# Kernel tuning notes

Measured on AMD Instinct MI355X. Metric: run time of the kernel, lower is better.

The kernel has to match this reference:

```python
import jax, jax.numpy as jnp
import numpy as np

B, S, D, H, C, E, V = 8, 2048, 1024, 512, 256, 64, 64


def setup_inputs() -> dict:
    key = jax.random.key(0)
    ks = jax.random.split(key, 40)
    ri = lambda i, hi: jax.random.randint(ks[i], (B, S), 0, hi).astype(jnp.int32)
    p = lambda i, shape: (jax.random.normal(ks[i], shape, jnp.float32) * 0.02)
    inp = {
        'h_x': jax.random.normal(ks[0], (B, S, D), jnp.float32),
        'h_y': jax.random.normal(ks[1], (B, S, D), jnp.float32),
        'x_mask': jnp.ones((B, S), jnp.int32),
        'y_mask': jnp.ones((B, S), jnp.int32),
        'src_token_dense_mask': ri(2, 2), 'src_token_sparse_mask': ri(3, 2),
        'src_token_inarc_type': ri(4, V), 'src_token_arc_head': ri(5, S),
        'src_token_depth': ri(6, 16), 'src_word_inarc_type': ri(7, V),
        'src_word_inarc_type_mask': ri(8, 2),
        'tgt_token_dense_mask': ri(9, 2), 'tgt_token_sparse_mask': ri(10, 2),
        'tgt_token_inarc_type': ri(11, V), 'tgt_token_arc_head': ri(12, S),
        'tgt_token_depth': ri(13, 16), 'tgt_word_inarc_type': ri(14, V),
        'tgt_word_inarc_type_mask': ri(15, 2),
        # src MLP [D->H->C], tgt MLP [D->H->C]
        'W1s': p(16, (D, H)), 'b1s': jnp.zeros((H,), jnp.float32),
        'W2s': p(17, (H, C)), 'b2s': jnp.zeros((C,), jnp.float32),
        'W1t': p(18, (D, H)), 'b1t': jnp.zeros((H,), jnp.float32),
        'W2t': p(19, (H, C)), 'b2t': jnp.zeros((C,), jnp.float32),
        # inarc edge embedding + GeneralConv params
        'emb': p(20, (V, E)),
        'W_msg': p(21, (C, C)), 'b_msg': jnp.zeros((C,), jnp.float32),
        'W_edge': p(22, (E, C)),
        'att': p(23, (C,)),
        'W_self': p(24, (C, C)), 'b_self': jnp.zeros((C,), jnp.float32),
        # axis_feature MLP [C->C]
        'Wf': p(25, (C, C)), 'bf': jnp.zeros((C,), jnp.float32),
    }
    return inp


def _mlp(h, W1, b1, W2, b2):
    return jax.nn.leaky_relu(h @ W1 + b1) @ W2 + b2


def _graph_side(h, dense_m, sparse_m, arc_head, word_type, word_mask,
                W1, b1, W2, b2, emb, W_msg, b_msg, W_edge, att, W_self, b_self, Wf, bf):
    Bn, Sn, _ = h.shape
    x = _mlp(h, W1, b1, W2, b2)                      # [B,S,C]
    N = Bn * Sn
    Cn = x.shape[-1]
    xg = x.reshape(N, Cn)                            # debatch -> nodes
    off = (jnp.arange(Bn, dtype=jnp.int32) * Sn)[:, None]
    src = (arc_head + off).reshape(N)                # global head index per token
    dst = jnp.arange(N, dtype=jnp.int32)             # one in-edge per token
    valid = (sparse_m * dense_m).reshape(N).astype(x.dtype)
    ef = emb[(word_type * word_mask).reshape(N)]     # [N,E] edge embeddings
    # GeneralConv: directed message with edge features + additive attention
    m = xg[src] @ W_msg + b_msg + ef @ W_edge        # [N,C] messages
    hd = xg @ W_msg + b_msg                          # dst-side term for attention
    logit = jax.nn.leaky_relu(((m + hd) * att).sum(-1))
    logit = jnp.where(valid > 0, logit, -1e9)
    emax = jax.ops.segment_max(logit, dst, num_segments=N)
    ex = jnp.exp(logit - emax[dst]) * valid
    den = jax.ops.segment_sum(ex, dst, num_segments=N)
    alpha = ex / (den[dst] + 1e-16)                  # softmax per destination node
    agg = jax.ops.segment_sum(m * alpha[:, None], dst, num_segments=N)
    out = xg @ W_self + b_self + agg                 # skip_linear
    out = out / jnp.maximum(jnp.linalg.norm(out, axis=-1, keepdims=True), 1e-12)
    r = out.reshape(Bn, Sn, Cn).mean(axis=1, keepdims=True)  # FeatureRepr mean
    return r @ Wf + bf                               # [B,1,C]


def reference(h_x, x_mask, src_token_dense_mask, src_token_sparse_mask,
              src_token_inarc_type, src_token_arc_head, src_token_depth,
              src_word_inarc_type, src_word_inarc_type_mask,
              h_y, y_mask, tgt_token_dense_mask, tgt_token_sparse_mask,
              tgt_token_inarc_type, tgt_token_arc_head, tgt_token_depth,
              tgt_word_inarc_type, tgt_word_inarc_type_mask,
              W1s, b1s, W2s, b2s, W1t, b1t, W2t, b2t,
              emb, W_msg, b_msg, W_edge, att, W_self, b_self, Wf, bf):
    src_repr = _graph_side(h_x, src_token_dense_mask, src_token_sparse_mask,
                           src_token_arc_head, src_word_inarc_type, src_word_inarc_type_mask,
                           W1s, b1s, W2s, b2s, emb, W_msg, b_msg, W_edge, att,
                           W_self, b_self, Wf, bf)
    tgt_repr = _graph_side(h_y, tgt_token_dense_mask, tgt_token_sparse_mask,
                           tgt_token_arc_head, tgt_word_inarc_type, tgt_word_inarc_type_mask,
                           W1t, b1t, W2t, b2t, emb, W_msg, b_msg, W_edge, att,
                           W_self, b_self, Wf, bf)
    return (src_repr, tgt_repr)
```

## Files before the change

### kernel.cpp

```cpp
#include <hip/hip_runtime.h>
#include <stdint.h>

#define SEQ   2048
#define NNODE 16384

typedef short  short8  __attribute__((ext_vector_type(8)));
typedef float  float4v __attribute__((ext_vector_type(4)));
typedef unsigned short u16;
typedef unsigned short u16x8 __attribute__((ext_vector_type(8)));
typedef short  short4v __attribute__((ext_vector_type(4)));

__device__ __forceinline__ float b2f(u16 u) {
    union { unsigned int i; float f; } x; x.i = ((unsigned int)u) << 16; return x.f;
}
__device__ __forceinline__ u16 f2b(float f) {
    union { float f; unsigned int i; } x; x.f = f;
    unsigned int u = x.i;
    unsigned int r = (u + 0x7fffu + ((u >> 16) & 1u)) >> 16;
    return (u16)r;
}

__device__ __forceinline__ void gld16(const void* g, void* l) {
    __builtin_amdgcn_global_load_lds(
        (const __attribute__((address_space(1))) void*)g,
        (__attribute__((address_space(3))) void*)l, 16, 0, 0);
}

struct GemmP {
    const void*  A[2];
    const u16*   B[2];
    const float* bias[2];
    u16*         out[2];
};

template <int MB>
__device__ __forceinline__ void mfma4(const short8* af, const short8* bq,
                                      float4v (*acc)[4]) {
#pragma unroll
    for (int mi = 0; mi < 4; ++mi)
#pragma unroll
        for (int ni = 0; ni < 4; ++ni)
            acc[MB + mi][ni] = __builtin_amdgcn_mfma_f32_16x16x32_bf16(
                af[mi], bq[ni], acc[MB + mi][ni], 0, 0, 0);
}

#define TILE_BODY(AC, BC, KN, AG, BG, ACV, PL, PC)                            \
    {                                                                         \
        short8 bq[4], af[4];                                                  \
        _Pragma("unroll") for (int ni = 0; ni < 4; ++ni)                      \
            bq[ni] = *(const short8*)((BC) + boff + ni * 512);                \
        _Pragma("unroll") for (int mi = 0; mi < 4; ++mi)                      \
            af[mi] = *(const short8*)((AC) + aoff + mi * 512);                \
        if constexpr (AF32) prefA32(KN, PL); else stageA16(KN, AG);           \
        __builtin_amdgcn_s_barrier();                                         \
        __builtin_amdgcn_s_setprio(1);                                        \
        mfma4<0>(af, bq, acc);                                                \
        __builtin_amdgcn_s_setprio(0);                                        \
        __builtin_amdgcn_s_barrier();                                         \
        _Pragma("unroll") for (int mi = 0; mi < 4; ++mi)                      \
            af[mi] = *(const short8*)((AC) + aoff + (4 + mi) * 512);          \
        stageB(KN, BG);                                                       \
        if constexpr (AF32) {                                                 \
            cvtWrite(PC, ACV);                                                \
            asm volatile("s_waitcnt lgkmcnt(0)" ::: "memory");                \
            asm volatile("s_waitcnt vmcnt(6)" ::: "memory");                  \
        } else {                                                              \
            asm volatile("s_waitcnt vmcnt(4)" ::: "memory");                  \
        }                                                                     \
        __builtin_amdgcn_s_barrier();                                         \
        __builtin_amdgcn_s_setprio(1);                                        \
        mfma4<4>(af, bq, acc);                                                \
        __builtin_amdgcn_s_setprio(0);                                        \
        __builtin_amdgcn_s_barrier();                                         \
    }

template <int ACT, int AF32>
__global__ __launch_bounds__(512, 2) void gemm8_k(GemmP p, int M, int N, int K) {
    __shared__ __align__(16) u16 smem[49152];

    const int z = blockIdx.z;
    const u16*   __restrict__ Bg   = p.B[z];
    const float* __restrict__ bias = p.bias[z];
    const u16*   __restrict__ A16  = (const u16*)p.A[z];
    const float* __restrict__ A32  = (const float*)p.A[z];

    const int mt  = blockIdx.x * 256;
    const int nt  = blockIdx.y * 256;
    const int tid = threadIdx.x;
    const int l   = tid & 63;
    const int w   = tid >> 6;
    const int wm  = (w >> 2) * 128;
    const int wn  = (w & 3) * 64;
    const int lr  = l & 15;
    const int lk  = l >> 4;
    (void)M;

    float4v acc[8][4] = {};
    float4v paA[4], paB[4];

    const int rm0 = tid >> 2;
    const int cc0 = tid & 3;
    const int gc0 = cc0 ^ (rm0 & 3) ^ ((rm0 >> 2) & 3);
    const int rm1 = rm0 + 128;

    u16* const As0 = smem;
    u16* const Bs0 = smem + 24576;

    auto stageA16 = [&](int k0, u16* dst) {
        gld16(A16 + (size_t)(mt + rm0) * K + k0 + gc0 * 8, dst + tid * 8);
        gld16(A16 + (size_t)(mt + rm1) * K + k0 + gc0 * 8, dst + (tid + 512) * 8);
    };
    auto stageB = [&](int k0, u16* dst) {
        gld16(Bg + (size_t)(nt + rm0) * K + k0 + gc0 * 8, dst + tid * 8);
        gld16(Bg + (size_t)(nt + rm1) * K + k0 + gc0 * 8, dst + (tid + 512) * 8);
    };
    auto prefA32 = [&](int k0, float4v* pa) {
        const float* s0 = A32 + (size_t)(mt + rm0) * K + k0 + gc0 * 8;
        const float* s1 = A32 + (size_t)(mt + rm1) * K + k0 + gc0 * 8;
        pa[0] = *(const float4v*)s0; pa[1] = *(const float4v*)(s0 + 4);
        pa[2] = *(const float4v*)s1; pa[3] = *(const float4v*)(s1 + 4);
    };
    auto cvtWrite = [&](const float4v* pa, u16* dst) {
        u16x8 r0, r1;
        r0[0]=f2b(pa[0][0]); r0[1]=f2b(pa[0][1]); r0[2]=f2b(pa[0][2]); r0[3]=f2b(pa[0][3]);
        r0[4]=f2b(pa[1][0]); r0[5]=f2b(pa[1][1]); r0[6]=f2b(pa[1][2]); r0[7]=f2b(pa[1][3]);
        r1[0]=f2b(pa[2][0]); r1[1]=f2b(pa[2][1]); r1[2]=f2b(pa[2][2]); r1[3]=f2b(pa[2][3]);
        r1[4]=f2b(pa[3][0]); r1[5]=f2b(pa[3][1]); r1[6]=f2b(pa[3][2]); r1[7]=f2b(pa[3][3]);
        *(u16x8*)(dst + tid * 8) = r0;
        *(u16x8*)(dst + (tid + 512) * 8) = r1;
    };

    const int fsl  = lk ^ (lr & 3) ^ ((lr >> 2) & 3);
    const int aoff = (wm + lr) * 32 + fsl * 8;
    const int boff = (wn + lr) * 32 + fsl * 8;

    const int KT = K >> 5;

    if constexpr (AF32) {
        float4v p0[4];
        prefA32(0, p0);
        stageB(0, Bs0);
        prefA32(32, paB);
        stageB(32, Bs0 + 8192);
        cvtWrite(p0, As0);
        asm volatile("s_waitcnt lgkmcnt(0)" ::: "memory");
        asm volatile("s_waitcnt vmcnt(6)" ::: "memory");
    } else {
        stageA16(0, As0);          stageB(0, Bs0);
        stageA16(32, As0 + 8192);  stageB(32, Bs0 + 8192);
        asm volatile("s_waitcnt vmcnt(4)" ::: "memory");
    }
    __builtin_amdgcn_s_barrier();

    int sc = 0;
    for (int kt = 0; kt < KT; kt += 2) {
        const int sc1 = (sc == 2) ? 0 : sc + 1;
        const int sc2 = (sc1 == 2) ? 0 : sc1 + 1;
        u16* Ae = As0 + sc  * 8192;  u16* Be = Bs0 + sc  * 8192;
        u16* Ao = As0 + sc1 * 8192;  u16* Bo = Bs0 + sc1 * 8192;
        u16* A2 = As0 + sc2 * 8192;  u16* B2 = Bs0 + sc2 * 8192;
        const int k2 = (kt + 2 < KT) ? (kt + 2) << 5 : 0;
        const int k3 = (kt + 3 < KT) ? (kt + 3) << 5 : 0;
        TILE_BODY(Ae, Be, k2, A2, B2, Ao, paA, paB)
        TILE_BODY(Ao, Bo, k3, Ae, Be, A2, paB, paA)
        sc = sc2;
    }

    __syncthreads();

    const int r0 = lk * 4;
    float bvv[4];
#pragma unroll
    for (int ni = 0; ni < 4; ++ni) bvv[ni] = bias[nt + wn + ni * 16 + lr];
    const int half = w >> 2;
#pragma unroll
    for (int pass = 0; pass < 2; ++pass) {
        if (half == pass) {
#pragma unroll
            for (int mi = 0; mi < 8; ++mi)
#pragma unroll
                for (int ni = 0; ni < 4; ++ni) {
                    const int lc = wn + ni * 16 + lr;
#pragma unroll
                    for (int r = 0; r < 4; ++r) {
                        float v = acc[mi][ni][r] + bvv[ni];
                        if (ACT) v = v > 0.f ? v : 0.01f * v;
                        smem[(mi * 16 + r0 + r) * 264 + lc] = f2b(v);
                    }
                }
        }
        __syncthreads();
#pragma unroll
        for (int it = 0; it < 8; ++it) {
            const int id  = it * 512 + tid;
            const int row = id >> 5, colc = id & 31;
            u16x8 vv = *(const u16x8*)(smem + (size_t)row * 264 + colc * 8);
            *(u16x8*)(p.out[z] + (size_t)(mt + pass * 128 + row) * N + nt + colc * 8) = vv;
        }
        __syncthreads();
    }
}

struct TP { const float* src[6]; u16* dst[6]; int K[6]; int N[6]; };

__global__ __launch_bounds__(256) void transpose_k(TP t) {
    __shared__ float tile[64][65];
    const int m = blockIdx.y;
    const int K = t.K[m], N = t.N[m];
    const int tn = N >> 6;
    const int ntiles = (K >> 6) * tn;
    const int bid = blockIdx.x;
    if (bid >= ntiles) return;
    const int k0 = (bid / tn) * 64, n0 = (bid % tn) * 64;
    const int tid = threadIdx.x;
#pragma unroll
    for (int pass = 0; pass < 4; ++pass) {
        int kk = pass * 16 + (tid >> 4);
        int nn = (tid & 15) * 4;
        float4v v = *(const float4v*)(t.src[m] + (size_t)(k0 + kk) * N + n0 + nn);
        tile[kk][nn + 0] = v[0]; tile[kk][nn + 1] = v[1];
        tile[kk][nn + 2] = v[2]; tile[kk][nn + 3] = v[3];
    }
    __syncthreads();
    const int n = tid >> 2, kc = (tid & 3) * 16;
    u16x8 a, b;
#pragma unroll
    for (int j = 0; j < 8; ++j) {
        a[j] = f2b(tile[kc + j][n]);
        b[j] = f2b(tile[kc + 8 + j][n]);
    }
    u16* d = t.dst[m] + (size_t)(n0 + n) * K + k0 + kc;
    *(u16x8*)d = a;
    *(u16x8*)(d + 8) = b;
}

__global__ void ew_k(const float* emb, const float* W_edge, float* EW) {
    const int t = blockIdx.x, c = threadIdx.x;
    float s = 0.f;
    for (int e = 0; e < 64; ++e)
        s += emb[t * 64 + e] * W_edge[e * 256 + c];
    EW[t * 256 + c] = s;
}

__global__ void bias_cat_k(const float* bmsg, const float* bself, float* bcat) {
    const int tid = threadIdx.x;
    bcat[tid]       = bmsg[tid];
    bcat[256 + tid] = bself[tid];
}

struct EpiP {
    const u16* xcat[2];
    const int* den[2]; const int* spa[2]; const int* arc[2];
    const int* wty[2]; const int* wma[2];
    const float* EW; float* racc;
};

__global__ __launch_bounds__(256) void epi_k(EpiP p) {
    __shared__ float part[4][256];
    const int bx    = blockIdx.x;
    const int side  = bx >> 9;
    const int local = bx & 511;
    const int base  = local * 32;
    const int b     = base >> 11;
    const int tid   = threadIdx.x;
    const int w = tid >> 6, l = tid & 63;

    const u16* __restrict__ xcat = p.xcat[side];

    float4v acc = {};
    for (int j = 0; j < 8; ++j) {
        const int i     = base + w * 8 + j;
        const int valid = p.den[side][i] * p.spa[side][i];
        const int srcn  = p.arc[side][i] + (i >> 11) * SEQ;
        const int t     = p.wty[side][i] * p.wma[side][i];
        short4v xs = *(const short4v*)(xcat + (size_t)i * 512 + 256 + l * 4);
        short4v xm = *(const short4v*)(xcat + (size_t)srcn * 512 + l * 4);
        float4v ew = *(const float4v*)(p.EW + (size_t)t * 256 + l * 4);
        const float vm = valid ? 1.f : 0.f;
        float4v v;
        v[0] = b2f((u16)xs[0]) + vm * (b2f((u16)xm[0]) + ew[0]);
        v[1] = b2f((u16)xs[1]) + vm * (b2f((u16)xm[1]) + ew[1]);
        v[2] = b2f((u16)xs[2]) + vm * (b2f((u16)xm[2]) + ew[2]);
        v[3] = b2f((u16)xs[3]) + vm * (b2f((u16)xm[3]) + ew[3]);
        float ss = v[0]*v[0] + v[1]*v[1] + v[2]*v[2] + v[3]*v[3];
        for (int m = 32; m >= 1; m >>= 1) ss += __shfl_xor(ss, m, 64);
        const float rn = 1.f / fmaxf(sqrtf(ss), 1e-12f);
        acc[0] += v[0] * rn; acc[1] += v[1] * rn;
        acc[2] += v[2] * rn; acc[3] += v[3] * rn;
    }
    part[w][l * 4 + 0] = acc[0];
    part[w][l * 4 + 1] = acc[1];
    part[w][l * 4 + 2] = acc[2];
    part[w][l * 4 + 3] = acc[3];
    __syncthreads();
    const float s = part[0][tid] + part[1][tid] + part[2][tid] + part[3][tid];
    atomicAdd(p.racc + ((size_t)side * 8 + b) * 256 + tid, s);
}

__global__ void fin_k(const float* racc, const float* Wf, const float* bfv,
                      float* out) {
    __shared__ float r[256];
    const int bid = blockIdx.x;
    const int tid = threadIdx.x;
    r[tid] = racc[bid * 256 + tid] * (1.f / 2048.f);
    __syncthreads();
    float s = bfv[tid];
    for (int k = 0; k < 256; ++k)
        s += r[k] * Wf[k * 256 + tid];
    out[bid * 256 + tid] = s;
}

extern "C" void kernel_launch(void* const* d_in, const int* in_sizes, int n_in,
                              void* d_out, int out_size, void* d_ws, size_t ws_size,
                              hipStream_t stream) {
    const float* h[2]   = {(const float*)d_in[0],  (const float*)d_in[1]};
    const int* den[2]   = {(const int*)d_in[4],  (const int*)d_in[11]};
    const int* spa[2]   = {(const int*)d_in[5],  (const int*)d_in[12]};
    const int* arc[2]   = {(const int*)d_in[7],  (const int*)d_in[14]};
    const int* wty[2]   = {(const int*)d_in[9],  (const int*)d_in[16]};
    const int* wma[2]   = {(const int*)d_in[10], (const int*)d_in[17]};
    const float* W1[2]  = {(const float*)d_in[18], (const float*)d_in[22]};
    const float* b1[2]  = {(const float*)d_in[19], (const float*)d_in[23]};
    const float* W2[2]  = {(const float*)d_in[20], (const float*)d_in[24]};
    const float* b2[2]  = {(const float*)d_in[21], (const float*)d_in[25]};
    const float* emb    = (const float*)d_in[26];
    const float* Wmsg   = (const float*)d_in[27];
    const float* bmsg   = (const float*)d_in[28];
    const float* Wedge  = (const float*)d_in[29];
    const float* Wself  = (const float*)d_in[31];
    const float* bself  = (const float*)d_in[32];
    const float* Wf     = (const float*)d_in[33];
    const float* bf_    = (const float*)d_in[34];

    char* ws = (char*)d_ws;
    size_t off = 0;
    auto alloc = [&](size_t bytes) -> void* {
        void* pp = ws + off; off += (bytes + 255) & ~(size_t)255; return pp;
    };
    u16*   x1    = (u16*)  alloc(2ull * NNODE * 512 * 2);
    u16*   xx    = (u16*)  alloc(2ull * NNODE * 256 * 2);
    u16*   xcat  = (u16*)  alloc(2ull * NNODE * 512 * 2);
    u16*   W1T   = (u16*)  alloc(2ull * 512 * 1024 * 2);
    u16*   W2T   = (u16*)  alloc(2ull * 256 * 512 * 2);
    u16*   WcatT = (u16*)  alloc(512 * 256 * 2);
    float* EW    = (float*)alloc(64 * 256 * 4);
    float* bcat  = (float*)alloc(512 * 4);
    float* racc  = (float*)alloc(2 * 8 * 256 * 4);

    TP tp;
    tp.src[0] = W1[0]; tp.dst[0] = W1T;              tp.K[0] = 1024; tp.N[0] = 512;
    tp.src[1] = W1[1]; tp.dst[1] = W1T + 512 * 1024; tp.K[1] = 1024; tp.N[1] = 512;
    tp.src[2] = W2[0]; tp.dst[2] = W2T;              tp.K[2] = 512;  tp.N[2] = 256;
    tp.src[3] = W2[1]; tp.dst[3] = W2T + 256 * 512;  tp.K[3] = 512;  tp.N[3] = 256;
    tp.src[4] = Wmsg;  tp.dst[4] = WcatT;            tp.K[4] = 256;  tp.N[4] = 256;
    tp.src[5] = Wself; tp.dst[5] = WcatT + 256*256;  tp.K[5] = 256;  tp.N[5] = 256;
    hipLaunchKernelGGL(transpose_k, dim3(128, 6), dim3(256), 0, stream, tp);
    hipLaunchKernelGGL(ew_k, dim3(64), dim3(256), 0, stream, emb, Wedge, EW);
    hipLaunchKernelGGL(bias_cat_k, dim3(1), dim3(256), 0, stream, bmsg, bself, bcat);
    hipMemsetAsync(racc, 0, 2 * 8 * 256 * 4, stream);

    GemmP g1 = {};
    g1.A[0] = h[0];  g1.A[1] = h[1];
    g1.B[0] = W1T;   g1.B[1] = W1T + 512 * 1024;
    g1.bias[0] = b1[0]; g1.bias[1] = b1[1];
    g1.out[0] = x1;  g1.out[1] = x1 + (size_t)NNODE * 512;
    hipLaunchKernelGGL((gemm8_k<1, 1>), dim3(64, 2, 2), dim3(512), 0, stream,
                       g1, NNODE, 512, 1024);

    GemmP g2 = {};
    g2.A[0] = x1;  g2.A[1] = x1 + (size_t)NNODE * 512;
    g2.B[0] = W2T; g2.B[1] = W2T + 256 * 512;
    g2.bias[0] = b2[0]; g2.bias[1] = b2[1];
    g2.out[0] = xx; g2.out[1] = xx + (size_t)NNODE * 256;
    hipLaunchKernelGGL((gemm8_k<0, 0>), dim3(64, 1, 2), dim3(512), 0, stream,
                       g2, NNODE, 256, 512);

    GemmP g3 = {};
    g3.A[0] = xx;    g3.A[1] = xx + (size_t)NNODE * 256;
    g3.B[0] = WcatT; g3.B[1] = WcatT;
    g3.bias[0] = bcat; g3.bias[1] = bcat;
    g3.out[0] = xcat;  g3.out[1] = xcat + (size_t)NNODE * 512;
    hipLaunchKernelGGL((gemm8_k<0, 0>), dim3(64, 2, 2), dim3(512), 0, stream,
                       g3, NNODE, 512, 256);

    EpiP ep;
    ep.xcat[0] = xcat; ep.xcat[1] = xcat + (size_t)NNODE * 512;
    for (int s = 0; s < 2; ++s) {
        ep.den[s] = den[s]; ep.spa[s] = spa[s]; ep.arc[s] = arc[s];
        ep.wty[s] = wty[s]; ep.wma[s] = wma[s];
    }
    ep.EW = EW; ep.racc = racc;
    hipLaunchKernelGGL(epi_k, dim3(1024), dim3(256), 0, stream, ep);

    hipLaunchKernelGGL(fin_k, dim3(16), dim3(256), 0, stream,
                       racc, Wf, bf_, (float*)d_out);
}
```

Baseline: 301.8 us.

## Software-pipeline LDS fragment reads across MFMA halves in bf16 GEMM loop

Restructures the GEMM main loop so that the LDS fragment reads for the next half-tile and the next k-tile are issued before the current MFMA block completes. This lets LDS latency hide behind matrix math instead of stalling at the start of each tile. The fp32-A path now converts and writes the prefetched registers one stage earlier, keeping a single prefetch buffer, and the loop drops two barriers per tile. In exchange it keeps more fragment registers live, and the reordered barriers and waitcnts have to stay correct for the three-stage ring buffer.

```diff
diff --git a/kernel.cpp b/kernel.cpp
--- a/kernel.cpp
+++ b/kernel.cpp
@@ -44,35 +44,13 @@
                 af[mi], bq[ni], acc[MB + mi][ni], 0, 0, 0);
 }
 
-#define TILE_BODY(AC, BC, KN, AG, BG, ACV, PL, PC)                            \
-    {                                                                         \
-        short8 bq[4], af[4];                                                  \
-        _Pragma("unroll") for (int ni = 0; ni < 4; ++ni)                      \
-            bq[ni] = *(const short8*)((BC) + boff + ni * 512);                \
-        _Pragma("unroll") for (int mi = 0; mi < 4; ++mi)                      \
-            af[mi] = *(const short8*)((AC) + aoff + mi * 512);                \
-        if constexpr (AF32) prefA32(KN, PL); else stageA16(KN, AG);           \
-        __builtin_amdgcn_s_barrier();                                         \
-        __builtin_amdgcn_s_setprio(1);                                        \
-        mfma4<0>(af, bq, acc);                                                \
-        __builtin_amdgcn_s_setprio(0);                                        \
-        __builtin_amdgcn_s_barrier();                                         \
-        _Pragma("unroll") for (int mi = 0; mi < 4; ++mi)                      \
-            af[mi] = *(const short8*)((AC) + aoff + (4 + mi) * 512);          \
-        stageB(KN, BG);                                                       \
-        if constexpr (AF32) {                                                 \
-            cvtWrite(PC, ACV);                                                \
-            asm volatile("s_waitcnt lgkmcnt(0)" ::: "memory");                \
-            asm volatile("s_waitcnt vmcnt(6)" ::: "memory");                  \
-        } else {                                                              \
-            asm volatile("s_waitcnt vmcnt(4)" ::: "memory");                  \
-        }                                                                     \
-        __builtin_amdgcn_s_barrier();                                         \
-        __builtin_amdgcn_s_setprio(1);                                        \
-        mfma4<4>(af, bq, acc);                                                \
-        __builtin_amdgcn_s_setprio(0);                                        \
-        __builtin_amdgcn_s_barrier();                                         \
-    }
+#define READ_BQ(Bs, bq)                                                       \
+    _Pragma("unroll") for (int ni = 0; ni < 4; ++ni)                          \
+        bq[ni] = *(const short8*)((Bs) + boff + ni * 512);
+
+#define READ_AF(As, half, af)                                                 \
+    _Pragma("unroll") for (int mi = 0; mi < 4; ++mi)                          \
+        af[mi] = *(const short8*)((As) + aoff + ((half) * 4 + mi) * 512);
 
 template <int ACT, int AF32>
 __global__ __launch_bounds__(512, 2) void gemm8_k(GemmP p, int M, int N, int K) {
@@ -96,7 +74,8 @@
     (void)M;
 
     float4v acc[8][4] = {};
-    float4v paA[4], paB[4];
+    float4v pa[4];
+    short8 bqE[4], bqO[4], af03[4], af47[4];
 
     const int rm0 = tid >> 2;
     const int cc0 = tid & 3;
@@ -114,13 +93,13 @@
         gld16(Bg + (size_t)(nt + rm0) * K + k0 + gc0 * 8, dst + tid * 8);
         gld16(Bg + (size_t)(nt + rm1) * K + k0 + gc0 * 8, dst + (tid + 512) * 8);
     };
-    auto prefA32 = [&](int k0, float4v* pa) {
+    auto prefA32 = [&](int k0) {
         const float* s0 = A32 + (size_t)(mt + rm0) * K + k0 + gc0 * 8;
         const float* s1 = A32 + (size_t)(mt + rm1) * K + k0 + gc0 * 8;
         pa[0] = *(const float4v*)s0; pa[1] = *(const float4v*)(s0 + 4);
         pa[2] = *(const float4v*)s1; pa[3] = *(const float4v*)(s1 + 4);
     };
-    auto cvtWrite = [&](const float4v* pa, u16* dst) {
+    auto cvtWrite = [&](u16* dst) {
         u16x8 r0, r1;
         r0[0]=f2b(pa[0][0]); r0[1]=f2b(pa[0][1]); r0[2]=f2b(pa[0][2]); r0[3]=f2b(pa[0][3]);
         r0[4]=f2b(pa[1][0]); r0[5]=f2b(pa[1][1]); r0[6]=f2b(pa[1][2]); r0[7]=f2b(pa[1][3]);
@@ -137,20 +116,22 @@
     const int KT = K >> 5;
 
     if constexpr (AF32) {
-        float4v p0[4];
-        prefA32(0, p0);
+        prefA32(0);
         stageB(0, Bs0);
-        prefA32(32, paB);
+        cvtWrite(As0);
+        prefA32(32);
         stageB(32, Bs0 + 8192);
-        cvtWrite(p0, As0);
+        cvtWrite(As0 + 8192);
+        prefA32(64);
         asm volatile("s_waitcnt lgkmcnt(0)" ::: "memory");
-        asm volatile("s_waitcnt vmcnt(6)" ::: "memory");
     } else {
         stageA16(0, As0);          stageB(0, Bs0);
         stageA16(32, As0 + 8192);  stageB(32, Bs0 + 8192);
         asm volatile("s_waitcnt vmcnt(4)" ::: "memory");
     }
     __builtin_amdgcn_s_barrier();
+    READ_BQ(Bs0, bqE)
+    READ_AF(As0, 0, af03)
 
     int sc = 0;
     for (int kt = 0; kt < KT; kt += 2) {
@@ -161,8 +142,52 @@
         u16* A2 = As0 + sc2 * 8192;  u16* B2 = Bs0 + sc2 * 8192;
         const int k2 = (kt + 2 < KT) ? (kt + 2) << 5 : 0;
         const int k3 = (kt + 3 < KT) ? (kt + 3) << 5 : 0;
-        TILE_BODY(Ae, Be, k2, A2, B2, Ao, paA, paB)
-        TILE_BODY(Ao, Bo, k3, Ae, Be, A2, paB, paA)
+        const int k4 = (kt + 4 < KT) ? (kt + 4) << 5 : 0;
+
+        __builtin_amdgcn_s_setprio(1);
+        mfma4<0>(af03, bqE, acc);
+        __builtin_amdgcn_s_setprio(0);
+        READ_AF(Ae, 1, af47)
+        __builtin_amdgcn_s_barrier();
+        if constexpr (AF32) {
+            cvtWrite(A2);
+            prefA32(k3);
+            stageB(k2, B2);
+            asm volatile("s_waitcnt vmcnt(6)" ::: "memory");
+        } else {
+            stageA16(k2, A2); stageB(k2, B2);
+            asm volatile("s_waitcnt vmcnt(4)" ::: "memory");
+        }
+        __builtin_amdgcn_s_barrier();
+        READ_BQ(Bo, bqO)
+        READ_AF(Ao, 0, af03)
+        __builtin_amdgcn_sched_barrier(0);
+        __builtin_amdgcn_s_setprio(1);
+        mfma4<4>(af47, bqE, acc);
+        __builtin_amdgcn_s_setprio(0);
+
+        __builtin_amdgcn_s_setprio(1);
+        mfma4<0>(af03, bqO, acc);
+        __builtin_amdgcn_s_setprio(0);
+        READ_AF(Ao, 1, af47)
+        __builtin_amdgcn_s_barrier();
+        if constexpr (AF32) {
+            cvtWrite(Ae);
+            prefA32(k4);
+            stageB(k3, Be);
+            asm volatile("s_waitcnt vmcnt(6)" ::: "memory");
+        } else {
+            stageA16(k3, Ae); stageB(k3, Be);
+            asm volatile("s_waitcnt vmcnt(4)" ::: "memory");
+        }
+        __builtin_amdgcn_s_barrier();
+        READ_BQ(B2, bqE)
+        READ_AF(A2, 0, af03)
+        __builtin_amdgcn_sched_barrier(0);
+        __builtin_amdgcn_s_setprio(1);
+        mfma4<4>(af47, bqO, acc);
+        __builtin_amdgcn_s_setprio(0);
+
         sc = sc2;
     }
 
```

After: 339.6 us. 12.5% more time.

## Fold W2 into message/self weights to merge two GEMMs into one

Applied to the files above, without the earlier changes.

Precomputes W23 = W2·[W_msg|W_self] and the combined bias b2·Wcat + bcat per side, then replaces the two back-to-back GEMMs (x1→xx, xx→xcat) with a single GEMM of K=512, N=512. This removes one kernel launch and the write and read of the intermediate xx tensor, but doubles the FLOPs of the merged GEMM compared with the old third GEMM, and it changes rounding because the intermediate bf16 step is gone. The vmcnt wait thresholds in the pipelined GEMM body are also raised to 8, allowing more outstanding loads before the barrier, which may be a correctness risk if the count no longer matches the number of in-flight loads. An unused b23_k kernel is left in.

```diff
diff --git a/kernel.cpp b/kernel.cpp
--- a/kernel.cpp
+++ b/kernel.cpp
@@ -63,9 +63,9 @@
         if constexpr (AF32) {                                                 \
             cvtWrite(PC, ACV);                                                \
             asm volatile("s_waitcnt lgkmcnt(0)" ::: "memory");                \
-            asm volatile("s_waitcnt vmcnt(6)" ::: "memory");                  \
+            asm volatile("s_waitcnt vmcnt(8)" ::: "memory");                  \
         } else {                                                              \
-            asm volatile("s_waitcnt vmcnt(4)" ::: "memory");                  \
+            asm volatile("s_waitcnt vmcnt(8)" ::: "memory");                  \
         }                                                                     \
         __builtin_amdgcn_s_barrier();                                         \
         __builtin_amdgcn_s_setprio(1);                                        \
@@ -144,11 +144,11 @@
         stageB(32, Bs0 + 8192);
         cvtWrite(p0, As0);
         asm volatile("s_waitcnt lgkmcnt(0)" ::: "memory");
-        asm volatile("s_waitcnt vmcnt(6)" ::: "memory");
+        asm volatile("s_waitcnt vmcnt(8)" ::: "memory");
     } else {
         stageA16(0, As0);          stageB(0, Bs0);
         stageA16(32, As0 + 8192);  stageB(32, Bs0 + 8192);
-        asm volatile("s_waitcnt vmcnt(4)" ::: "memory");
+        asm volatile("s_waitcnt vmcnt(8)" ::: "memory");
     }
     __builtin_amdgcn_s_barrier();
 
@@ -242,10 +242,58 @@
     EW[t * 256 + c] = s;
 }
 
-__global__ void bias_cat_k(const float* bmsg, const float* bself, float* bcat) {
-    const int tid = threadIdx.x;
-    bcat[tid]       = bmsg[tid];
-    bcat[256 + tid] = bself[tid];
+struct WmP { const float* W2[2]; const float* Wmsg; const float* Wself;
+             float* W23[2]; };
+
+__global__ __launch_bounds__(512) void wmul_k(WmP q) {
+    __shared__ float w2[16][256];
+    const int side = blockIdx.y;
+    const int k0 = blockIdx.x * 16;
+    const int n = threadIdx.x;
+    const float* __restrict__ W2 = q.W2[side];
+    for (int i = threadIdx.x; i < 4096; i += 512)
+        w2[i >> 8][i & 255] = W2[(size_t)(k0 + (i >> 8)) * 256 + (i & 255)];
+    __syncthreads();
+    const float* __restrict__ Wc = (n < 256) ? q.Wmsg : q.Wself;
+    const int nn = n & 255;
+    float acc[16] = {};
+    for (int c = 0; c < 256; ++c) {
+        const float wc = Wc[c * 256 + nn];
+#pragma unroll
+        for (int kk = 0; kk < 16; ++kk) acc[kk] += w2[kk][c] * wc;
+    }
+    for (int kk = 0; kk < 16; ++kk)
+        q.W23[side][(size_t)(k0 + kk) * 512 + n] = acc[kk];
+}
+
+struct B23P { const float* b2[2]; const float* bmsg; const float* bself;
+              float* b23; };
+
+__global__ void b23_k(B23P q) {
+    const int side = blockIdx.x;
+    const int n = threadIdx.x;
+    const float* __restrict__ Wc = (n < 256) ? q.bmsg : q.bself;
+    (void)Wc;
+    const float* __restrict__ Wcat = nullptr;
+    (void)Wcat;
+    const float* __restrict__ b2 = q.b2[side];
+    float s = (n < 256) ? q.bmsg[n] : q.bself[n - 256];
+    q.b23[side * 512 + n] = s;
+}
+
+struct B23WP { const float* b2[2]; const float* bmsg; const float* bself;
+               const float* Wmsg; const float* Wself; float* b23; };
+
+__global__ void b23w_k(B23WP q) {
+    const int side = blockIdx.x;
+    const int n = threadIdx.x;
+    const float* __restrict__ W = (n < 256) ? q.Wmsg : q.Wself;
+    const int nn = n & 255;
+    const float* __restrict__ b2 = q.b2[side];
+    float s = (n < 256) ? q.bmsg[nn] : q.bself[nn];
+    for (int c = 0; c < 256; ++c)
+        s += b2[c] * W[c * 256 + nn];
+    q.b23[side * 512 + n] = s;
 }
 
 struct EpiP {
@@ -338,25 +386,37 @@
         void* pp = ws + off; off += (bytes + 255) & ~(size_t)255; return pp;
     };
     u16*   x1    = (u16*)  alloc(2ull * NNODE * 512 * 2);
-    u16*   xx    = (u16*)  alloc(2ull * NNODE * 256 * 2);
     u16*   xcat  = (u16*)  alloc(2ull * NNODE * 512 * 2);
     u16*   W1T   = (u16*)  alloc(2ull * 512 * 1024 * 2);
-    u16*   W2T   = (u16*)  alloc(2ull * 256 * 512 * 2);
-    u16*   WcatT = (u16*)  alloc(512 * 256 * 2);
+    float* W23   = (float*)alloc(2ull * 512 * 512 * 4);
+    u16*   W23T  = (u16*)  alloc(2ull * 512 * 512 * 2);
     float* EW    = (float*)alloc(64 * 256 * 4);
-    float* bcat  = (float*)alloc(512 * 4);
+    float* b23   = (float*)alloc(2 * 512 * 4);
     float* racc  = (float*)alloc(2 * 8 * 256 * 4);
 
-    TP tp;
+    TP tp = {};
     tp.src[0] = W1[0]; tp.dst[0] = W1T;              tp.K[0] = 1024; tp.N[0] = 512;
     tp.src[1] = W1[1]; tp.dst[1] = W1T + 512 * 1024; tp.K[1] = 1024; tp.N[1] = 512;
-    tp.src[2] = W2[0]; tp.dst[2] = W2T;              tp.K[2] = 512;  tp.N[2] = 256;
-    tp.src[3] = W2[1]; tp.dst[3] = W2T + 256 * 512;  tp.K[3] = 512;  tp.N[3] = 256;
-    tp.src[4] = Wmsg;  tp.dst[4] = WcatT;            tp.K[4] = 256;  tp.N[4] = 256;
-    tp.src[5] = Wself; tp.dst[5] = WcatT + 256*256;  tp.K[5] = 256;  tp.N[5] = 256;
-    hipLaunchKernelGGL(transpose_k, dim3(128, 6), dim3(256), 0, stream, tp);
+    hipLaunchKernelGGL(transpose_k, dim3(128, 2), dim3(256), 0, stream, tp);
     hipLaunchKernelGGL(ew_k, dim3(64), dim3(256), 0, stream, emb, Wedge, EW);
-    hipLaunchKernelGGL(bias_cat_k, dim3(1), dim3(256), 0, stream, bmsg, bself, bcat);
+
+    WmP wq;
+    wq.W2[0] = W2[0]; wq.W2[1] = W2[1];
+    wq.Wmsg = Wmsg; wq.Wself = Wself;
+    wq.W23[0] = W23; wq.W23[1] = W23 + 512 * 512;
+    hipLaunchKernelGGL(wmul_k, dim3(32, 2), dim3(512), 0, stream, wq);
+
+    TP tp2 = {};
+    tp2.src[0] = W23;            tp2.dst[0] = W23T;            tp2.K[0] = 512; tp2.N[0] = 512;
+    tp2.src[1] = W23 + 512*512;  tp2.dst[1] = W23T + 512*512;  tp2.K[1] = 512; tp2.N[1] = 512;
+    hipLaunchKernelGGL(transpose_k, dim3(64, 2), dim3(256), 0, stream, tp2);
+
+    B23WP bq;
+    bq.b2[0] = b2[0]; bq.b2[1] = b2[1];
+    bq.bmsg = bmsg; bq.bself = bself;
+    bq.Wmsg = Wmsg; bq.Wself = Wself;
+    bq.b23 = b23;
+    hipLaunchKernelGGL(b23w_k, dim3(2), dim3(512), 0, stream, bq);
     hipMemsetAsync(racc, 0, 2 * 8 * 256 * 4, stream);
 
     GemmP g1 = {};
@@ -367,21 +427,13 @@
     hipLaunchKernelGGL((gemm8_k<1, 1>), dim3(64, 2, 2), dim3(512), 0, stream,
                        g1, NNODE, 512, 1024);
 
-    GemmP g2 = {};
-    g2.A[0] = x1;  g2.A[1] = x1 + (size_t)NNODE * 512;
-    g2.B[0] = W2T; g2.B[1] = W2T + 256 * 512;
-    g2.bias[0] = b2[0]; g2.bias[1] = b2[1];
-    g2.out[0] = xx; g2.out[1] = xx + (size_t)NNODE * 256;
-    hipLaunchKernelGGL((gemm8_k<0, 0>), dim3(64, 1, 2), dim3(512), 0, stream,
-                       g2, NNODE, 256, 512);
-
-    GemmP g3 = {};
-    g3.A[0] = xx;    g3.A[1] = xx + (size_t)NNODE * 256;
-    g3.B[0] = WcatT; g3.B[1] = WcatT;
-    g3.bias[0] = bcat; g3.bias[1] = bcat;
-    g3.out[0] = xcat;  g3.out[1] = xcat + (size_t)NNODE * 512;
+    GemmP g23 = {};
+    g23.A[0] = x1;   g23.A[1] = x1 + (size_t)NNODE * 512;
+    g23.B[0] = W23T; g23.B[1] = W23T + 512 * 512;
+    g23.bias[0] = b23; g23.bias[1] = b23 + 512;
+    g23.out[0] = xcat; g23.out[1] = xcat + (size_t)NNODE * 512;
     hipLaunchKernelGGL((gemm8_k<0, 0>), dim3(64, 2, 2), dim3(512), 0, stream,
-                       g3, NNODE, 512, 256);
+                       g23, NNODE, 512, 512);
 
     EpiP ep;
     ep.xcat[0] = xcat; ep.xcat[1] = xcat + (size_t)NNODE * 512;
```

Result: slower. 338.2 us (+12.1%).

## Add 256x128-tile bf16 GEMM kernel for second and third GEMMs, relax vmcnt waits

Applied to the files above, without the earlier changes.

Adds a new gemmt_k kernel that uses 256x128 output tiles with K-step 64, an XOR-swizzled LDS layout, triple buffering and blockIdx swizzling. The bf16-input GEMMs (MLP layer 2 and the concatenated message/self projection) now use it, which doubles the number of blocks for better CU occupancy. The existing gemm8_k's vmcnt waits are loosened to 8 so more global loads stay in flight. This risks a correctness hazard if the waits no longer cover all outstanding loads. The ew_k loop also gets four independent accumulators.

```diff
diff --git a/kernel.cpp b/kernel.cpp
--- a/kernel.cpp
+++ b/kernel.cpp
@@ -63,9 +63,9 @@
         if constexpr (AF32) {                                                 \
             cvtWrite(PC, ACV);                                                \
             asm volatile("s_waitcnt lgkmcnt(0)" ::: "memory");                \
-            asm volatile("s_waitcnt vmcnt(6)" ::: "memory");                  \
+            asm volatile("s_waitcnt vmcnt(8)" ::: "memory");                  \
         } else {                                                              \
-            asm volatile("s_waitcnt vmcnt(4)" ::: "memory");                  \
+            asm volatile("s_waitcnt vmcnt(8)" ::: "memory");                  \
         }                                                                     \
         __builtin_amdgcn_s_barrier();                                         \
         __builtin_amdgcn_s_setprio(1);                                        \
@@ -144,11 +144,11 @@
         stageB(32, Bs0 + 8192);
         cvtWrite(p0, As0);
         asm volatile("s_waitcnt lgkmcnt(0)" ::: "memory");
-        asm volatile("s_waitcnt vmcnt(6)" ::: "memory");
+        asm volatile("s_waitcnt vmcnt(8)" ::: "memory");
     } else {
         stageA16(0, As0);          stageB(0, Bs0);
         stageA16(32, As0 + 8192);  stageB(32, Bs0 + 8192);
-        asm volatile("s_waitcnt vmcnt(4)" ::: "memory");
+        asm volatile("s_waitcnt vmcnt(8)" ::: "memory");
     }
     __builtin_amdgcn_s_barrier();
 
@@ -201,6 +201,123 @@
     }
 }
 
+#define FPHASE(ASL, BSL, KH, STAGE, DO_VM)                                    \
+    {                                                                         \
+        short8 af[4], bq[4];                                                  \
+        _Pragma("unroll") for (int mi = 0; mi < 4; ++mi)                      \
+            af[mi] = *(const short8*)((ASL) +                                 \
+                (size_t)(wm * 64 + mi * 16 + lr) * 64 +                       \
+                (((KH) * 4 + lk) ^ (lr & 7)) * 8);                            \
+        _Pragma("unroll") for (int ni = 0; ni < 4; ++ni)                      \
+            bq[ni] = *(const short8*)((BSL) +                                 \
+                (size_t)(wn * 64 + ni * 16 + lr) * 64 +                       \
+                (((KH) * 4 + lk) ^ (lr & 7)) * 8);                            \
+        STAGE;                                                                \
+        if (DO_VM) asm volatile("s_waitcnt vmcnt(6)" ::: "memory");           \
+        __builtin_amdgcn_s_barrier();                                         \
+        asm volatile("s_waitcnt lgkmcnt(0)" ::: "memory");                    \
+        __builtin_amdgcn_s_setprio(1);                                        \
+        _Pragma("unroll") for (int mi = 0; mi < 4; ++mi)                      \
+            _Pragma("unroll") for (int ni = 0; ni < 4; ++ni)                  \
+                acc[mi][ni] = __builtin_amdgcn_mfma_f32_16x16x32_bf16(        \
+                    af[mi], bq[ni], acc[mi][ni], 0, 0, 0);                    \
+        __builtin_amdgcn_s_setprio(0);                                        \
+        __builtin_amdgcn_s_barrier();                                         \
+    }
+
+template <int ACT>
+__global__ __launch_bounds__(512, 2) void gemmt_k(GemmP p, int M, int N, int K) {
+    __shared__ __align__(16) u16 smem[73728];
+
+    const int z = blockIdx.z;
+    const u16*   __restrict__ Ag   = (const u16*)p.A[z];
+    const u16*   __restrict__ Bg   = p.B[z];
+    const float* __restrict__ bias = p.bias[z];
+
+    const int nblk = gridDim.x;
+    const int cpx  = nblk >> 3;
+    const int flat = blockIdx.x;
+    const int swz  = (flat & 7) * cpx + (flat >> 3);
+    const int nbn  = N >> 7;
+    const int mt   = (swz / nbn) * 256;
+    const int nt   = (swz % nbn) * 128;
+
+    const int tid = threadIdx.x;
+    const int l   = tid & 63;
+    const int w   = tid >> 6;
+    const int wm  = w >> 1;
+    const int wn  = w & 1;
+    const int lr  = l & 15;
+    const int lk  = l >> 4;
+    (void)M;
+
+    float4v acc[4][4] = {};
+
+    const int srow   = tid >> 3;
+    const int gchunk = (tid & 7) ^ (srow & 7);
+
+    u16* const As0 = smem;
+    u16* const Bs0 = smem + 49152;
+
+    auto stageA = [&](int k0, u16* dst) {
+#pragma unroll
+        for (int i = 0; i < 4; ++i)
+            gld16(Ag + (size_t)(mt + srow + 64 * i) * K + k0 + gchunk * 8,
+                  dst + (size_t)(tid + 512 * i) * 8);
+    };
+    auto stageB = [&](int k0, u16* dst) {
+#pragma unroll
+        for (int i = 0; i < 2; ++i)
+            gld16(Bg + (size_t)(nt + srow + 64 * i) * K + k0 + gchunk * 8,
+                  dst + (size_t)(tid + 512 * i) * 8);
+    };
+
+    const int NT = K >> 6;
+
+    stageA(0, As0);          stageB(0, Bs0);
+    stageA(64, As0 + 16384); stageB(64, Bs0 + 8192);
+    asm volatile("s_waitcnt vmcnt(6)" ::: "memory");
+    __builtin_amdgcn_s_barrier();
+
+    int sc = 0;
+    for (int T = 0; T < NT; ++T) {
+        const int sc2 = (sc >= 1) ? sc - 1 : 2;
+        u16* Ac = As0 + sc  * 16384;  u16* Bc = Bs0 + sc  * 8192;
+        u16* A2 = As0 + sc2 * 16384;  u16* B2 = Bs0 + sc2 * 8192;
+        const int k2 = (T + 2 < NT) ? (T + 2) << 6 : 0;
+        FPHASE(Ac, Bc, 0, stageA(k2, A2), 0)
+        FPHASE(Ac, Bc, 1, stageB(k2, B2), 1)
+        sc = (sc == 2) ? 0 : sc + 1;
+    }
+
+    __syncthreads();
+
+    const int er0 = lk * 4;
+    float bvv[4];
+#pragma unroll
+    for (int ni = 0; ni < 4; ++ni) bvv[ni] = bias[nt + wn * 64 + ni * 16 + lr];
+#pragma unroll
+    for (int mi = 0; mi < 4; ++mi)
+#pragma unroll
+        for (int ni = 0; ni < 4; ++ni) {
+            const int lc = wn * 64 + ni * 16 + lr;
+#pragma unroll
+            for (int r = 0; r < 4; ++r) {
+                float v = acc[mi][ni][r] + bvv[ni];
+                if (ACT) v = v > 0.f ? v : 0.01f * v;
+                smem[(size_t)(wm * 64 + mi * 16 + er0 + r) * 136 + lc] = f2b(v);
+            }
+        }
+    __syncthreads();
+#pragma unroll
+    for (int it = 0; it < 8; ++it) {
+        const int id  = it * 512 + tid;
+        const int row = id >> 4, colc = id & 15;
+        u16x8 vv = *(const u16x8*)(smem + (size_t)row * 136 + colc * 8);
+        *(u16x8*)(p.out[z] + (size_t)(mt + row) * N + nt + colc * 8) = vv;
+    }
+}
+
 struct TP { const float* src[6]; u16* dst[6]; int K[6]; int N[6]; };
 
 __global__ __launch_bounds__(256) void transpose_k(TP t) {
@@ -236,10 +353,14 @@
 
 __global__ void ew_k(const float* emb, const float* W_edge, float* EW) {
     const int t = blockIdx.x, c = threadIdx.x;
-    float s = 0.f;
-    for (int e = 0; e < 64; ++e)
-        s += emb[t * 64 + e] * W_edge[e * 256 + c];
-    EW[t * 256 + c] = s;
+    float p0 = 0.f, p1 = 0.f, p2 = 0.f, p3 = 0.f;
+    for (int e = 0; e < 64; e += 4) {
+        p0 += emb[t * 64 + e + 0] * W_edge[(e + 0) * 256 + c];
+        p1 += emb[t * 64 + e + 1] * W_edge[(e + 1) * 256 + c];
+        p2 += emb[t * 64 + e + 2] * W_edge[(e + 2) * 256 + c];
+        p3 += emb[t * 64 + e + 3] * W_edge[(e + 3) * 256 + c];
+    }
+    EW[t * 256 + c] = (p0 + p1) + (p2 + p3);
 }
 
 __global__ void bias_cat_k(const float* bmsg, const float* bself, float* bcat) {
@@ -372,7 +493,7 @@
     g2.B[0] = W2T; g2.B[1] = W2T + 256 * 512;
     g2.bias[0] = b2[0]; g2.bias[1] = b2[1];
     g2.out[0] = xx; g2.out[1] = xx + (size_t)NNODE * 256;
-    hipLaunchKernelGGL((gemm8_k<0, 0>), dim3(64, 1, 2), dim3(512), 0, stream,
+    hipLaunchKernelGGL((gemmt_k<0>), dim3(128, 1, 2), dim3(512), 0, stream,
                        g2, NNODE, 256, 512);
 
     GemmP g3 = {};
@@ -380,7 +501,7 @@
     g3.B[0] = WcatT; g3.B[1] = WcatT;
     g3.bias[0] = bcat; g3.bias[1] = bcat;
     g3.out[0] = xcat;  g3.out[1] = xcat + (size_t)NNODE * 512;
-    hipLaunchKernelGGL((gemm8_k<0, 0>), dim3(64, 2, 2), dim3(512), 0, stream,
+    hipLaunchKernelGGL((gemmt_k<0>), dim3(256, 1, 2), dim3(512), 0, stream,
                        g3, NNODE, 512, 256);
 
     EpiP ep;
```

Result: no change. 302.5 us (+0.3%).
